# Optimization experiments

Hardware: AMD Instinct MI355X
Metric: run time of the kernel (lower is better)

## Reference

```python
import jax, jax.numpy as jnp
import numpy as np

N, D = 2048, 64
H, W = 128, 128
NEAR, RADIUS_CLIP, BLUR = 0.01, 3.0, 0.3
A_MIN, A_MAX = 1.0 / 255.0, 0.999


def setup_inputs():
    key = jax.random.key(0)
    k = jax.random.split(key, 6)
    xy = jax.random.uniform(k[0], (N, 2), minval=-1.2, maxval=1.2)
    zz = jax.random.uniform(k[1], (N, 1), minval=3.0, maxval=5.0)
    means = jnp.concatenate([xy, zz], axis=1).astype(jnp.float32)
    quats = jax.random.normal(k[2], (N, 4), dtype=jnp.float32)
    scales = jax.random.normal(k[3], (N, 3), dtype=jnp.float32) * 0.3 - 2.2  # log-scales
    opacities = jax.random.normal(k[4], (N,), dtype=jnp.float32) * 0.5 + 1.0  # logits
    gs_features = jax.random.normal(k[5], (N, D), dtype=jnp.float32) * 0.5
    c2o = jnp.eye(4, dtype=jnp.float32)
    K = jnp.array([[200.0, 0.0, 64.0], [0.0, 200.0, 64.0], [0.0, 0.0, 1.0]], dtype=jnp.float32)
    return dict(means=means, quats=quats, scales=scales, opacities=opacities,
                gs_features=gs_features, c2o=c2o, K=K, width=W, height=H)


def _quat_to_rot(q):
    q = q / jnp.linalg.norm(q, axis=-1, keepdims=True)
    w, x, y, z = q[:, 0], q[:, 1], q[:, 2], q[:, 3]
    r0 = jnp.stack([1 - 2 * (y * y + z * z), 2 * (x * y - w * z), 2 * (x * z + w * y)], -1)
    r1 = jnp.stack([2 * (x * y + w * z), 1 - 2 * (x * x + z * z), 2 * (y * z - w * x)], -1)
    r2 = jnp.stack([2 * (x * z - w * y), 2 * (y * z + w * x), 1 - 2 * (x * x + y * y)], -1)
    return jnp.stack([r0, r1, r2], -2)  # [N,3,3]


def _rasterize(means, quats, log_scales, opac_logits, colors, viewmat, K, width, height):
    Rv, tv = viewmat[:3, :3], viewmat[:3, 3]
    fx, fy, cx, cy = K[0, 0], K[1, 1], K[0, 2], K[1, 2]
    mc = means @ Rv.T + tv                      # camera-space means [N,3]
    x, y, z = mc[:, 0], mc[:, 1], mc[:, 2]
    # 3D covariance Sigma = R S S^T R^T, rotated into camera frame
    M = _quat_to_rot(quats) * jnp.exp(log_scales)[:, None, :]
    cov_w = M @ jnp.swapaxes(M, 1, 2)           # [N,3,3]
    cov_c = jnp.einsum('ij,njk,lk->nil', Rv, cov_w, Rv)
    # perspective (EWA) Jacobian [N,2,3]
    rz = 1.0 / z
    zero = jnp.zeros_like(z)
    J = jnp.stack([jnp.stack([fx * rz, zero, -fx * x * rz * rz], -1),
                   jnp.stack([zero, fy * rz, -fy * y * rz * rz], -1)], -2)
    cov2d = jnp.einsum('nij,njk,nlk->nil', J, cov_c, J)
    a = cov2d[:, 0, 0] + BLUR
    b = cov2d[:, 0, 1]
    c = cov2d[:, 1, 1] + BLUR
    det = a * c - b * b
    cA, cB, cC = c / det, -b / det, a / det     # conic = inverse 2D covariance
    mx = fx * x * rz + cx
    my = fy * y * rz + cy
    # cull: behind near plane, degenerate, or projected 3-sigma radius below radius_clip
    lam_max = 0.5 * (a + c) + jnp.sqrt(jnp.maximum(0.25 * (a - c) ** 2 + b * b, 1e-12))
    radius = 3.0 * jnp.sqrt(lam_max)
    valid = (z > NEAR) & (det > 0) & (radius > RADIUS_CLIP)
    opac = jax.nn.sigmoid(opac_logits)
    # global front-to-back depth order (single camera)
    order = jnp.argsort(z)
    mx, my, cA, cB, cC = mx[order], my[order], cA[order], cB[order], cC[order]
    opac, valid, colors = opac[order], valid[order], colors[order]
    # per pixel-gaussian evaluation, [H,W,N]
    px = jnp.arange(width, dtype=means.dtype) + 0.5
    py = jnp.arange(height, dtype=means.dtype) + 0.5
    dx = px[None, :, None] - mx[None, None, :]
    dy = py[:, None, None] - my[None, None, :]
    sigma = 0.5 * (cA * dx * dx + cC * dy * dy) + cB * dx * dy
    alpha = jnp.minimum(opac * jnp.exp(-sigma), A_MAX)
    alpha = jnp.where((sigma >= 0) & valid & (alpha >= A_MIN), alpha, 0.0)
    # front-to-back alpha compositing: exclusive transmittance cumprod
    Tcum = jnp.cumprod(1.0 - alpha, axis=-1)
    T_excl = jnp.concatenate([jnp.ones_like(Tcum[..., :1]), Tcum[..., :-1]], axis=-1)
    out = jnp.einsum('hwn,nd->hwd', alpha * T_excl, colors)
    return out[None]  # [1,H,W,D]


def reference(means, quats, scales, opacities, gs_features, c2o, K, width, height):
    viewmat = jnp.linalg.inv(c2o)
    return _rasterize(means, quats, scales, opacities, gs_features, viewmat, K, width, height)
```

## Files before the change

### kernel.cpp

```cpp
#include <hip/hip_runtime.h>

constexpr int NG  = 2048;
constexpr int DF  = 64;
constexpr int IW  = 128;
constexpr int IH  = 128;
constexpr int NZ  = 8;
constexpr int RB  = 1024;
constexpr int CAP = 1024;

#define P_NEAR 0.01f
#define P_BLUR 0.3f
#define P_AMIN (1.0f/255.0f)
#define P_AMAX 0.999f

constexpr int L_T    = 0;
constexpr int L_CNT  = 512;
constexpr int L_SIDX = 528;
constexpr int L_OVL  = L_SIDX + CAP;
constexpr int L_PRM  = L_OVL;
constexpr int L_KEYS = L_PRM + CAP * 8;
constexpr int L_ACC  = L_OVL;
constexpr int ACC_ST = 66;
constexpr int L_TOTAL = L_OVL + NZ * 64 * ACC_ST;

__device__ inline void invert4x4(const float* m, float* inv) {
    inv[0]  =  m[5]*m[10]*m[15] - m[5]*m[11]*m[14] - m[9]*m[6]*m[15] + m[9]*m[7]*m[14] + m[13]*m[6]*m[11] - m[13]*m[7]*m[10];
    inv[4]  = -m[4]*m[10]*m[15] + m[4]*m[11]*m[14] + m[8]*m[6]*m[15] - m[8]*m[7]*m[14] - m[12]*m[6]*m[11] + m[12]*m[7]*m[10];
    inv[8]  =  m[4]*m[9]*m[15]  - m[4]*m[11]*m[13] - m[8]*m[5]*m[15] + m[8]*m[7]*m[13] + m[12]*m[5]*m[11] - m[12]*m[7]*m[9];
    inv[12] = -m[4]*m[9]*m[14]  + m[4]*m[10]*m[13] + m[8]*m[5]*m[14] - m[8]*m[6]*m[13] - m[12]*m[5]*m[10] + m[12]*m[6]*m[9];
    inv[1]  = -m[1]*m[10]*m[15] + m[1]*m[11]*m[14] + m[9]*m[2]*m[15] - m[9]*m[3]*m[14] - m[13]*m[2]*m[11] + m[13]*m[3]*m[10];
    inv[5]  =  m[0]*m[10]*m[15] - m[0]*m[11]*m[14] - m[8]*m[2]*m[15] + m[8]*m[3]*m[14] + m[12]*m[2]*m[11] - m[12]*m[3]*m[10];
    inv[9]  = -m[0]*m[9]*m[15]  + m[0]*m[11]*m[13] + m[8]*m[1]*m[15] - m[8]*m[3]*m[13] - m[12]*m[1]*m[11] + m[12]*m[3]*m[9];
    inv[13] =  m[0]*m[9]*m[14]  - m[0]*m[10]*m[13] - m[8]*m[1]*m[14] + m[8]*m[2]*m[13] + m[12]*m[1]*m[10] - m[12]*m[2]*m[9];
    inv[2]  =  m[1]*m[6]*m[15]  - m[1]*m[7]*m[14]  - m[5]*m[2]*m[15] + m[5]*m[3]*m[14] + m[13]*m[2]*m[7]  - m[13]*m[3]*m[6];
    inv[6]  = -m[0]*m[6]*m[15]  + m[0]*m[7]*m[14]  + m[4]*m[2]*m[15] - m[4]*m[3]*m[14] - m[12]*m[2]*m[7]  + m[12]*m[3]*m[6];
    inv[10] =  m[0]*m[5]*m[15]  - m[0]*m[7]*m[13]  - m[4]*m[1]*m[15] + m[4]*m[3]*m[13] + m[12]*m[1]*m[7]  - m[12]*m[3]*m[5];
    inv[14] = -m[0]*m[5]*m[14]  + m[0]*m[6]*m[13]  + m[4]*m[1]*m[14] - m[4]*m[2]*m[13] - m[12]*m[1]*m[6]  + m[12]*m[2]*m[5];
    inv[3]  = -m[1]*m[6]*m[11]  + m[1]*m[7]*m[10]  + m[5]*m[2]*m[11] - m[5]*m[3]*m[10] - m[9]*m[2]*m[7]   + m[9]*m[3]*m[6];
    inv[7]  =  m[0]*m[6]*m[11]  - m[0]*m[7]*m[10]  - m[4]*m[2]*m[11] + m[4]*m[3]*m[10] + m[8]*m[2]*m[7]   - m[8]*m[3]*m[6];
    inv[11] = -m[0]*m[5]*m[11]  + m[0]*m[7]*m[9]   + m[4]*m[1]*m[11] - m[4]*m[3]*m[9]  - m[8]*m[1]*m[7]   + m[8]*m[3]*m[5];
    inv[15] =  m[0]*m[5]*m[10]  - m[0]*m[6]*m[9]   - m[4]*m[1]*m[10] + m[4]*m[2]*m[9]  + m[8]*m[1]*m[6]   - m[8]*m[2]*m[5];
    float det = m[0]*inv[0] + m[1]*inv[4] + m[2]*inv[8] + m[3]*inv[12];
    det = 1.0f / det;
    #pragma unroll
    for (int i = 0; i < 16; ++i) inv[i] *= det;
}

__global__ __launch_bounds__(RB, 4) void fused_render_kernel(
    const float* __restrict__ means,  const float* __restrict__ quats,
    const float* __restrict__ scales, const float* __restrict__ opac_logits,
    const float* __restrict__ colors, const float* __restrict__ c2o,
    const float* __restrict__ Kmat,   float* __restrict__ out)
{
    extern __shared__ float lds[];
    int*                cnt  = (int*)(lds + L_CNT);
    int*                sidx = (int*)(lds + L_SIDX);
    unsigned long long* keys = (unsigned long long*)(lds + L_KEYS);
    float4*             prm4 = (float4*)(lds + L_PRM);

    const int tid  = threadIdx.x;
    const int lane = tid & 63;
    const int wv16 = tid >> 6;
    const int sz   = wv16 >> 1;
    const int hh   = wv16 & 1;
    const int tile = blockIdx.x;
    const int tx = (tile & 15) * 8;
    const int ty = (tile >> 4) * 8;
    const float px = tx + (lane & 7) + 0.5f;
    const float py = ty + (lane >> 3) + 0.5f;
    const float cxt = tx + 4.0f, cyt = ty + 4.0f;

    if (tid == 0) *cnt = 0;
    __syncthreads();

    {
        float inv[16];
        {
            float m[16];
            #pragma unroll
            for (int t = 0; t < 16; ++t) m[t] = c2o[t];
            invert4x4(m, inv);
        }
        const float fx = Kmat[0], fy = Kmat[4], cx = Kmat[2], cy = Kmat[5];

        #pragma unroll
        for (int c = 0; c < NG / RB; ++c) {
            const int g = c * RB + tid;
            float mx = means[g*3+0], my = means[g*3+1], mz = means[g*3+2];
            float X = inv[0]*mx + inv[1]*my + inv[2]*mz  + inv[3];
            float Y = inv[4]*mx + inv[5]*my + inv[6]*mz  + inv[7];
            float Z = inv[8]*mx + inv[9]*my + inv[10]*mz + inv[11];

            float qw = quats[g*4+0], qx = quats[g*4+1], qy = quats[g*4+2], qz = quats[g*4+3];
            float qn = rsqrtf(qw*qw + qx*qx + qy*qy + qz*qz);
            qw *= qn; qx *= qn; qy *= qn; qz *= qn;
            float R00 = 1.f - 2.f*(qy*qy + qz*qz), R01 = 2.f*(qx*qy - qw*qz), R02 = 2.f*(qx*qz + qw*qy);
            float R10 = 2.f*(qx*qy + qw*qz), R11 = 1.f - 2.f*(qx*qx + qz*qz), R12 = 2.f*(qy*qz - qw*qx);
            float R20 = 2.f*(qx*qz - qw*qy), R21 = 2.f*(qy*qz + qw*qx), R22 = 1.f - 2.f*(qx*qx + qy*qy);

            float s0 = expf(scales[g*3+0]), s1 = expf(scales[g*3+1]), s2 = expf(scales[g*3+2]);
            float M00 = R00*s0, M01 = R01*s1, M02 = R02*s2;
            float M10 = R10*s0, M11 = R11*s1, M12 = R12*s2;
            float M20 = R20*s0, M21 = R21*s1, M22 = R22*s2;

            float V00 = M00*M00 + M01*M01 + M02*M02;
            float V01 = M00*M10 + M01*M11 + M02*M12;
            float V02 = M00*M20 + M01*M21 + M02*M22;
            float V11 = M10*M10 + M11*M11 + M12*M12;
            float V12 = M10*M20 + M11*M21 + M12*M22;
            float V22 = M20*M20 + M21*M21 + M22*M22;

            float Rv[3][3] = {{inv[0],inv[1],inv[2]},{inv[4],inv[5],inv[6]},{inv[8],inv[9],inv[10]}};
            float Vm[3][3] = {{V00,V01,V02},{V01,V11,V12},{V02,V12,V22}};
            float Tm[3][3], C[3][3];
            #pragma unroll
            for (int r = 0; r < 3; ++r)
                #pragma unroll
                for (int cc = 0; cc < 3; ++cc)
                    Tm[r][cc] = Rv[r][0]*Vm[0][cc] + Rv[r][1]*Vm[1][cc] + Rv[r][2]*Vm[2][cc];
            #pragma unroll
            for (int r = 0; r < 3; ++r)
                #pragma unroll
                for (int cc = 0; cc < 3; ++cc)
                    C[r][cc] = Tm[r][0]*Rv[cc][0] + Tm[r][1]*Rv[cc][1] + Tm[r][2]*Rv[cc][2];

            float rz = 1.0f / Z;
            float j00 = fx*rz, j02 = -fx*X*rz*rz;
            float j11 = fy*rz, j12 = -fy*Y*rz*rz;

            float c00 = j00*j00*C[0][0] + 2.f*j00*j02*C[0][2] + j02*j02*C[2][2];
            float c01 = j00*j11*C[0][1] + j00*j12*C[0][2] + j02*j11*C[1][2] + j02*j12*C[2][2];
            float c11 = j11*j11*C[1][1] + 2.f*j11*j12*C[1][2] + j12*j12*C[2][2];

            float a = c00 + P_BLUR;
            float b = c01;
            float cc_ = c11 + P_BLUR;
            float det = a*cc_ - b*b;

            float pmx = fx*X*rz + cx;
            float pmy = fy*Y*rz + cy;

            float lam = 0.5f*(a + cc_) + sqrtf(fmaxf(0.25f*(a - cc_)*(a - cc_) + b*b, 1e-12f));
            float radius = 3.0f * sqrtf(lam);
            bool valid = (Z > P_NEAR) && (det > 0.0f) && (radius > 3.0f);

            float op = 1.0f / (1.0f + expf(-opac_logits[g]));

            bool sel = false;
            float cA = 0.f, cB = 0.f, cC2 = 0.f;
            if (valid) {
                float rdet = 1.0f / det;
                cA = cc_ * rdet; cB = -b * rdet; cC2 = a * rdet;
                float smax = logf(255.0f * op);
                if (smax > 0.f) {
                    float rx = sqrtf(2.f * a   * smax) * 1.0001f + 1e-3f;
                    float ry = sqrtf(2.f * cc_ * smax) * 1.0001f + 1e-3f;
                    sel = (fabsf(pmx - cxt) <= rx + 3.5f) && (fabsf(pmy - cyt) <= ry + 3.5f);
                }
            }

            unsigned long long m = __ballot(sel);
            int wbase = 0;
            if (lane == 0 && m) wbase = atomicAdd(cnt, (int)__popcll(m));
            wbase = __shfl(wbase, 0);
            if (sel) {
                int pos = wbase + (int)__popcll(m & ((1ull << lane) - 1ull));
                if (pos < CAP) {
                    prm4[pos*2]   = make_float4(pmx, pmy, cA, cB);
                    prm4[pos*2+1] = make_float4(cC2, op, __int_as_float(g), 0.f);
                    keys[pos] = ((unsigned long long)__float_as_uint(Z) << 32) | (unsigned)g;
                }
            }
        }
    }
    __syncthreads();
    int L = *cnt;
    if (L > CAP) L = CAP;

    {
        int padL = (L + 1) & ~1;
        if (tid < padL - L) keys[L + tid] = ~0ull;
        __syncthreads();
        const ulonglong2* k2 = (const ulonglong2*)keys;
        if (tid < L) {
            unsigned long long kk = keys[tid];
            int rank = 0;
            #pragma unroll 2
            for (int c = 0; c < padL / 2; ++c) {
                ulonglong2 q = k2[c];
                rank += (q.x < kk) + (q.y < kk);
            }
            sidx[rank] = tid;
        }
    }
    __syncthreads();

    float acc[32];
    #pragma unroll
    for (int f = 0; f < 32; ++f) acc[f] = 0.f;
    float T = 1.0f;

    {
        const int r0 = (sz * L) >> 3;
        const int r1 = ((sz + 1) * L) >> 3;
        const float4* cph = (const float4*)colors + hh * 8;
        if (r1 > r0) {
            int k = sidx[r0];
            float4 e0 = prm4[k*2], e1 = prm4[k*2+1];
            for (int r = r0; r < r1; ++r) {
                int kn = (r + 1 < r1) ? sidx[r + 1] : k;
                float4 n0 = prm4[kn*2], n1 = prm4[kn*2+1];

                float dx = px - e0.x, dy = py - e0.y;
                float sig = 0.5f*(e0.z*dx*dx + e1.x*dy*dy) + e0.w*dx*dy;
                float al = fminf(e1.y * __expf(-sig), P_AMAX);
                al = (sig >= 0.f && al >= P_AMIN) ? al : 0.f;

                if (__ballot(al > 0.f)) {
                    float wv = T * al;
                    const float4* crow = cph + (size_t)(unsigned)__float_as_int(e1.z) * 16;
                    #pragma unroll
                    for (int q = 0; q < 8; ++q) {
                        float4 cv = crow[q];
                        acc[4*q+0] = fmaf(wv, cv.x, acc[4*q+0]);
                        acc[4*q+1] = fmaf(wv, cv.y, acc[4*q+1]);
                        acc[4*q+2] = fmaf(wv, cv.z, acc[4*q+2]);
                        acc[4*q+3] = fmaf(wv, cv.w, acc[4*q+3]);
                    }
                    T *= (1.f - al);
                    if (!__ballot(T >= 1e-6f)) break;
                }
                e0 = n0; e1 = n1; k = kn;
            }
        }
    }

    if (hh == 0) lds[L_T + sz*64 + lane] = T;
    __syncthreads();
    {
        float* ab = lds + L_ACC + (size_t)(sz * 64 + lane) * ACC_ST + hh * 32;
        #pragma unroll
        for (int q = 0; q < 16; ++q)
            *(float2*)(ab + 2*q) = make_float2(acc[2*q], acc[2*q+1]);
    }
    __syncthreads();

    {
        int p  = tid >> 4;
        int f0 = (tid & 15) * 4;
        float r0, r1, r2, r3;
        const float* ab = lds + L_ACC + (size_t)((NZ-1)*64 + p) * ACC_ST + f0;
        { float2 u = *(const float2*)ab, v = *(const float2*)(ab + 2);
          r0 = u.x; r1 = u.y; r2 = v.x; r3 = v.y; }
        #pragma unroll
        for (int s = NZ - 2; s >= 0; --s) {
            float Ts = lds[L_T + s*64 + p];
            const float* as_ = lds + L_ACC + (size_t)(s*64 + p) * ACC_ST + f0;
            float2 u = *(const float2*)as_, v = *(const float2*)(as_ + 2);
            r0 = fmaf(Ts, r0, u.x); r1 = fmaf(Ts, r1, u.y);
            r2 = fmaf(Ts, r2, v.x); r3 = fmaf(Ts, r3, v.y);
        }
        int pyg = ty + (p >> 3), pxg = tx + (p & 7);
        float* op_ = out + (size_t)(pyg * IW + pxg) * DF + f0;
        *(float4*)op_ = make_float4(r0, r1, r2, r3);
    }
}

extern "C" void kernel_launch(void* const* d_in, const int* in_sizes, int n_in,
                              void* d_out, int out_size, void* d_ws, size_t ws_size,
                              hipStream_t stream) {
    const float* means  = (const float*)d_in[0];
    const float* quats  = (const float*)d_in[1];
    const float* scales = (const float*)d_in[2];
    const float* opac   = (const float*)d_in[3];
    const float* colors = (const float*)d_in[4];
    const float* c2o    = (const float*)d_in[5];
    const float* Kmat   = (const float*)d_in[6];
    float* out = (float*)d_out;
    (void)d_ws; (void)ws_size;

    (void)hipFuncSetAttribute((const void*)fused_render_kernel,
                              hipFuncAttributeMaxDynamicSharedMemorySize,
                              L_TOTAL * 4);

    fused_render_kernel<<<IH*IW/64, RB, L_TOTAL*4, stream>>>(
        means, quats, scales, opac, colors, c2o, Kmat, out);
}
```

Baseline: 115.4 us.

## Replace O(L^2) rank sort with bucketed counting sort plus per-bucket insertion sort

The per-tile depth sort used to rank each key against every other key, which costs O(L^2) LDS reads per tile. It is replaced by a min/max reduction over depth, a 256-bin histogram, a prefix scan, a scatter into buckets and an insertion sort inside each bucket. This cuts the comparison work but adds many block-wide barriers and an atomic scatter, and the insertion sort can be serial if depths cluster into a few buckets. LDS use grows with the new scratch arrays, which may overlap the existing accumulation region.

```diff
diff --git a/kernel.cpp b/kernel.cpp
--- a/kernel.cpp
+++ b/kernel.cpp
@@ -7,6 +7,7 @@
 constexpr int NZ  = 8;
 constexpr int RB  = 1024;
 constexpr int CAP = 1024;
+constexpr int NBK = 256;
 
 #define P_NEAR 0.01f
 #define P_BLUR 0.3f
@@ -19,6 +20,11 @@
 constexpr int L_OVL  = L_SIDX + CAP;
 constexpr int L_PRM  = L_OVL;
 constexpr int L_KEYS = L_PRM + CAP * 8;
+constexpr int L_KS2  = L_KEYS + CAP * 2;
+constexpr int L_HIST = L_KS2 + CAP * 2;
+constexpr int L_STRT = L_HIST + NBK;
+constexpr int L_CURS = L_STRT + NBK;
+constexpr int L_SCN  = L_CURS + NBK;
 constexpr int L_ACC  = L_OVL;
 constexpr int ACC_ST = 66;
 constexpr int L_TOTAL = L_OVL + NZ * 64 * ACC_ST;
@@ -56,6 +62,11 @@
     int*                cnt  = (int*)(lds + L_CNT);
     int*                sidx = (int*)(lds + L_SIDX);
     unsigned long long* keys = (unsigned long long*)(lds + L_KEYS);
+    unsigned long long* ks2  = (unsigned long long*)(lds + L_KS2);
+    int*                hist = (int*)(lds + L_HIST);
+    int*                strt = (int*)(lds + L_STRT);
+    int*                curs = (int*)(lds + L_CURS);
+    int*                scn  = (int*)(lds + L_SCN);
     float4*             prm4 = (float4*)(lds + L_PRM);
 
     const int tid  = threadIdx.x;
@@ -178,19 +189,71 @@
     if (L > CAP) L = CAP;
 
     {
-        int padL = (L + 1) & ~1;
-        if (tid < padL - L) keys[L + tid] = ~0ull;
+        float zl = 1e30f, zh = -1e30f;
+        if (tid < L) {
+            float z = __uint_as_float((unsigned)(keys[tid] >> 32));
+            zl = z; zh = z;
+        }
+        #pragma unroll
+        for (int o = 32; o; o >>= 1) {
+            zl = fminf(zl, __shfl_down(zl, o));
+            zh = fmaxf(zh, __shfl_down(zh, o));
+        }
+        if (lane == 0) { lds[L_SCN + wv16] = zl; lds[L_SCN + 16 + wv16] = zh; }
+    }
+    __syncthreads();
+    if (tid == 0) {
+        float a = lds[L_SCN], b = lds[L_SCN + 16];
+        for (int i = 1; i < 16; ++i) {
+            a = fminf(a, lds[L_SCN + i]); b = fmaxf(b, lds[L_SCN + 16 + i]);
+        }
+        lds[L_SCN + 32] = a; lds[L_SCN + 33] = b;
+    }
+    __syncthreads();
+    const float zmin = lds[L_SCN + 32];
+    const float zmax = lds[L_SCN + 33];
+    const float binv = (zmax > zmin) ? ((float)NBK / (zmax - zmin)) * 0.999999f : 0.f;
+    __syncthreads();
+
+    if (tid < NBK) { hist[tid] = 0; curs[tid] = 0; }
+    __syncthreads();
+    int myb = 0; unsigned long long myk = 0;
+    if (tid < L) {
+        myk = keys[tid];
+        float z = __uint_as_float((unsigned)(myk >> 32));
+        myb = (int)((z - zmin) * binv);
+        myb = max(0, min(myb, NBK - 1));
+        atomicAdd(&hist[myb], 1);
+    }
+    __syncthreads();
+
+    if (tid < NBK) scn[tid] = hist[tid];
+    __syncthreads();
+    for (int o = 1; o < NBK; o <<= 1) {
+        int t = (tid < NBK && tid >= o) ? scn[tid - o] : 0;
         __syncthreads();
-        const ulonglong2* k2 = (const ulonglong2*)keys;
-        if (tid < L) {
-            unsigned long long kk = keys[tid];
-            int rank = 0;
-            #pragma unroll 2
-            for (int c = 0; c < padL / 2; ++c) {
-                ulonglong2 q = k2[c];
-                rank += (q.x < kk) + (q.y < kk);
+        if (tid < NBK) scn[tid] += t;
+        __syncthreads();
+    }
+    if (tid < NBK) strt[tid] = scn[tid] - hist[tid];
+    __syncthreads();
+
+    if (tid < L) {
+        int pos = strt[myb] + atomicAdd(&curs[myb], 1);
+        ks2[pos]  = myk;
+        sidx[pos] = tid;
+    }
+    __syncthreads();
+
+    if (tid < NBK) {
+        int s = strt[tid], e = s + hist[tid];
+        for (int i = s + 1; i < e; ++i) {
+            unsigned long long k = ks2[i]; int sl = sidx[i];
+            int j = i - 1;
+            while (j >= s && ks2[j] > k) {
+                ks2[j+1] = ks2[j]; sidx[j+1] = sidx[j]; --j;
             }
-            sidx[rank] = tid;
+            ks2[j+1] = k; sidx[j+1] = sl;
         }
     }
     __syncthreads();
```

Measured after the change: 115.5 us. Within noise of the previous version (+0.1%).
